# Kernel tuning notes

Hardware: AMD Instinct MI355X
Metric: run time of the kernel (lower is better)

## Reference

```python
import jax, jax.numpy as jnp
import numpy as np

B, C_IN, H, W = 2048, 192, 19, 19
G1, P1 = 32, 32

def setup_inputs() -> dict:
    key = jax.random.key(0)
    ks = jax.random.split(key, 10)
    inputs = jax.random.normal(ks[0], (B, C_IN, H, W), dtype=jnp.float32)
    # binary validity mask (most points valid), plus its per-sample sum
    mask = (jax.random.uniform(ks[1], (B, 1, H, W)) > 0.1).astype(jnp.float32)
    mask_sum_hw = jnp.sum(mask, axis=(2, 3), keepdims=True)  # [B,1,1,1]
    s = 0.05
    return {
        "inputs": inputs,
        "mask": mask,
        "mask_sum_hw": mask_sum_hw,
        "w1p": jax.random.normal(ks[2], (P1, C_IN), dtype=jnp.float32) * s,
        "b1p": jnp.zeros((P1,), jnp.float32),
        "w1g": jax.random.normal(ks[3], (G1, C_IN), dtype=jnp.float32) * s,
        "b1g": jnp.zeros((G1,), jnp.float32),
        "beta_g": jnp.zeros((1, G1, 1, 1), jnp.float32),
        "w_lin": jax.random.normal(ks[4], (P1, 3 * G1), dtype=jnp.float32) * s,
        "b_lin": jnp.zeros((P1,), jnp.float32),
        "beta2": jnp.zeros((1, P1, 1, 1), jnp.float32),
        "w2p": jax.random.normal(ks[5], (1, P1), dtype=jnp.float32) * s,
        "b2p": jnp.zeros((1,), jnp.float32),
    }

def _conv1x1(x, w, b):
    # x: [B,C,H,W], w: [O,C] -> [B,O,H,W]
    return jnp.einsum('bchw,oc->bohw', x, w) + b[None, :, None, None]

def _gpool(x, mask, mask_sum_hw):
    # x: [B,G,H,W]; returns [B,3G,1,1]
    off = (jnp.sqrt(mask_sum_hw) - 28.0) / 10.0
    mean = jnp.sum(x, axis=(2, 3), keepdims=True) / mask_sum_hw
    mx = jnp.max(x + (mask - 1.0), axis=(2, 3), keepdims=True)
    return jnp.concatenate([mean, mean * off, mx], axis=1)

def reference(inputs, mask, mask_sum_hw, w1p, b1p, w1g, b1g, beta_g,
              w_lin, b_lin, beta2, w2p, b2p):
    b, _, h, w = inputs.shape
    outp = _conv1x1(inputs, w1p, b1p)                      # [B,P1,H,W]
    outg = _conv1x1(inputs, w1g, b1g)                      # [B,G1,H,W]
    outg = (outg + beta_g) * mask                          # NormMask (no gamma)
    outg = jax.nn.gelu(outg, approximate=False)            # torch GELU = exact erf
    outg = _gpool(outg, mask, mask_sum_hw)                 # [B,3G1,1,1]
    outg = outg.reshape(b, -1) @ w_lin.T + b_lin           # [B,P1]
    outp = outp + outg[:, :, None, None]
    outp = (outp + beta2) * mask                           # NormMask
    outp = jax.nn.gelu(outp, approximate=False)
    outp = _conv1x1(outp, w2p, b2p)                        # [B,1,H,W]
    outp = outp - (1.0 - mask) * 5000.0
    outp = jax.nn.log_softmax(outp.reshape(b, -1), axis=1)
    return outp.reshape(b, h, w)
```

## Files before the change

kernel.cpp:

```cpp
#include <hip/hip_runtime.h>
#include <math.h>

#define NB   2048
#define CIN  192
#define HW   361
#define NTH  512
#define WPAD 200

typedef float f32x4 __attribute__((ext_vector_type(4)));
typedef short s16x8 __attribute__((ext_vector_type(8)));

__device__ __forceinline__ unsigned short f2bf(float f) {
    unsigned int u = __float_as_uint(f);
    u += 0x7FFFu + ((u >> 16) & 1u);
    return (unsigned short)(u >> 16);
}

__device__ __forceinline__ float gelu_exact(float x) {
    return 0.5f * x * (1.0f + erff(x * 0.70710678118654752f));
}

__global__ __launch_bounds__(NTH)
void policy_head_mfma(const float* __restrict__ inputs,
                      const float* __restrict__ mask,
                      const float* __restrict__ mask_sum,
                      const float* __restrict__ w1p, const float* __restrict__ b1p,
                      const float* __restrict__ w1g, const float* __restrict__ b1g,
                      const float* __restrict__ beta_g,
                      const float* __restrict__ w_lin, const float* __restrict__ b_lin,
                      const float* __restrict__ beta2,
                      const float* __restrict__ w2p, const float* __restrict__ b2p,
                      float* __restrict__ out) {
    __shared__ unsigned short wlds[64 * WPAD];
    __shared__ float small[160];
    __shared__ float redA[32 * 8];
    __shared__ float redB[32 * 8];
    __shared__ float pooled[96];
    __shared__ float linout[32];

    const int tid = threadIdx.x;
    const int b   = blockIdx.x;

    for (int i = tid; i < 64 * CIN; i += NTH) {
        int o = i / CIN, c = i - o * CIN;
        float wv = (o < 32) ? w1p[o * CIN + c] : w1g[(o - 32) * CIN + c];
        wlds[o * WPAD + c] = f2bf(wv);
    }
    if (tid < 32)       small[tid] = b1p[tid];
    else if (tid < 64)  small[tid] = b1g[tid - 32];
    else if (tid < 96)  small[tid] = beta_g[tid - 64];
    else if (tid < 128) small[tid] = beta2[tid - 96];
    else if (tid < 160) small[tid] = w2p[tid - 128];
    __syncthreads();

    const int w    = tid >> 6;
    const int lane = tid & 63;
    const int g4   = lane >> 4;
    const int c16  = lane & 15;

    int   px[3], pxc[3];
    float mv[3];
    bool  valid[3];
    #pragma unroll
    for (int nt = 0; nt < 3; ++nt) {
        px[nt]    = w * 48 + nt * 16 + c16;
        valid[nt] = (px[nt] < HW);
        pxc[nt]   = valid[nt] ? px[nt] : (HW - 1);
        mv[nt]    = valid[nt] ? mask[(size_t)b * HW + px[nt]] : 0.f;
    }

    const float* xb = inputs + (size_t)b * (CIN * HW);

    f32x4 acc[4][3];
    #pragma unroll
    for (int mt = 0; mt < 4; ++mt)
        #pragma unroll
        for (int nt = 0; nt < 3; ++nt)
            acc[mt][nt] = (f32x4){0.f, 0.f, 0.f, 0.f};

    for (int kk = 0; kk < 6; ++kk) {
        s16x8 a[4];
        #pragma unroll
        for (int mt = 0; mt < 4; ++mt)
            a[mt] = *(const s16x8*)&wlds[(mt * 16 + c16) * WPAD + kk * 32 + 8 * g4];

        #pragma unroll
        for (int nt = 0; nt < 3; ++nt) {
            const float* xp = xb + (size_t)(kk * 32 + 8 * g4) * HW + pxc[nt];
            float xv[8];
            #pragma unroll
            for (int i = 0; i < 8; ++i) xv[i] = xp[i * HW];
            s16x8 bf;
            #pragma unroll
            for (int i = 0; i < 8; ++i) bf[i] = (short)f2bf(xv[i]);
            #pragma unroll
            for (int mt = 0; mt < 4; ++mt)
                acc[mt][nt] = __builtin_amdgcn_mfma_f32_16x16x32_bf16(a[mt], bf, acc[mt][nt], 0, 0, 0);
        }
    }

    const float ms  = mask_sum[b];
    const float off = (sqrtf(ms) - 28.0f) * 0.1f;

    #pragma unroll
    for (int mt = 2; mt < 4; ++mt) {
        #pragma unroll
        for (int r = 0; r < 4; ++r) {
            int og = (mt - 2) * 16 + g4 * 4 + r;
            float bb = small[32 + og] + small[64 + og];
            float s = 0.f, mx = -1e30f;
            #pragma unroll
            for (int nt = 0; nt < 3; ++nt) {
                float v = gelu_exact((acc[mt][nt][r] + bb) * mv[nt]);
                if (!valid[nt]) v = 0.f;
                s += v;
                float cand = valid[nt] ? (v + mv[nt] - 1.f) : -1e30f;
                mx = fmaxf(mx, cand);
            }
            #pragma unroll
            for (int o = 1; o < 16; o <<= 1) {
                s += __shfl_xor(s, o, 64);
                mx = fmaxf(mx, __shfl_xor(mx, o, 64));
            }
            if (c16 == 0) { redA[og * 8 + w] = s; redB[og * 8 + w] = mx; }
        }
    }
    __syncthreads();

    if (tid < 32) {
        float s = 0.f, mx = -1e30f;
        #pragma unroll
        for (int j = 0; j < 8; ++j) {
            s += redA[tid * 8 + j];
            mx = fmaxf(mx, redB[tid * 8 + j]);
        }
        float mean = s / ms;
        pooled[tid]      = mean;
        pooled[32 + tid] = mean * off;
        pooled[64 + tid] = mx;
    }
    __syncthreads();

    if (tid < 32) {
        float a = b_lin[tid];
        #pragma unroll
        for (int j = 0; j < 96; ++j) a = fmaf(pooled[j], w_lin[tid * 96 + j], a);
        linout[tid] = a;
    }
    __syncthreads();

    float pv[3] = {0.f, 0.f, 0.f};
    #pragma unroll
    for (int mt = 0; mt < 2; ++mt) {
        #pragma unroll
        for (int r = 0; r < 4; ++r) {
            int op = mt * 16 + g4 * 4 + r;
            float bb = small[op] + linout[op] + small[96 + op];
            float wo = small[128 + op];
            #pragma unroll
            for (int nt = 0; nt < 3; ++nt)
                pv[nt] += gelu_exact((acc[mt][nt][r] + bb) * mv[nt]) * wo;
        }
    }
    const float b2 = b2p[0];
    float logit[3];
    #pragma unroll
    for (int nt = 0; nt < 3; ++nt) {
        float t = pv[nt];
        t += __shfl_xor(t, 16, 64);
        t += __shfl_xor(t, 32, 64);
        logit[nt] = t + b2 - (1.f - mv[nt]) * 5000.f;
    }

    float lmax = -1e30f;
    #pragma unroll
    for (int nt = 0; nt < 3; ++nt)
        if (valid[nt]) lmax = fmaxf(lmax, logit[nt]);
    #pragma unroll
    for (int o = 1; o < 64; o <<= 1) lmax = fmaxf(lmax, __shfl_xor(lmax, o, 64));
    if (lane == 0) redA[w] = lmax;
    __syncthreads();
    float gmax = -1e30f;
    #pragma unroll
    for (int j = 0; j < 8; ++j) gmax = fmaxf(gmax, redA[j]);

    float es = 0.f;
    #pragma unroll
    for (int nt = 0; nt < 3; ++nt)
        if (valid[nt] && g4 == 0) es += expf(logit[nt] - gmax);
    #pragma unroll
    for (int o = 1; o < 64; o <<= 1) es += __shfl_xor(es, o, 64);
    if (lane == 0) redB[w] = es;
    __syncthreads();
    float tot = 0.f;
    #pragma unroll
    for (int j = 0; j < 8; ++j) tot += redB[j];
    const float lt = logf(tot) + gmax;

    if (g4 == 0) {
        #pragma unroll
        for (int nt = 0; nt < 3; ++nt)
            if (valid[nt]) out[(size_t)b * HW + px[nt]] = logit[nt] - lt;
    }
}

extern "C" void kernel_launch(void* const* d_in, const int* in_sizes, int n_in,
                              void* d_out, int out_size, void* d_ws, size_t ws_size,
                              hipStream_t stream) {
    const float* inputs   = (const float*)d_in[0];
    const float* mask     = (const float*)d_in[1];
    const float* mask_sum = (const float*)d_in[2];
    const float* w1p      = (const float*)d_in[3];
    const float* b1p      = (const float*)d_in[4];
    const float* w1g      = (const float*)d_in[5];
    const float* b1g      = (const float*)d_in[6];
    const float* beta_g   = (const float*)d_in[7];
    const float* w_lin    = (const float*)d_in[8];
    const float* b_lin    = (const float*)d_in[9];
    const float* beta2    = (const float*)d_in[10];
    const float* w2p      = (const float*)d_in[11];
    const float* b2p      = (const float*)d_in[12];
    float* out = (float*)d_out;

    policy_head_mfma<<<dim3(NB), dim3(NTH), 0, stream>>>(
        inputs, mask, mask_sum, w1p, b1p, w1g, b1g, beta_g,
        w_lin, b_lin, beta2, w2p, b2p, out);
}
```

Measured before the change: 176.7 us.

## Prefetch next K-slice of inputs, use tanh GELU approximation and fast intrinsics

Software-pipelines the global loads of input activations: each iteration converts the previously loaded slice to bf16 and issues the loads for the next slice before the MFMAs, to hide memory latency. It also replaces the exact erf GELU with a tanh-style approximation via __expf, switches expf/logf to fast intrinsics, uses the library bf16 conversion, and sets launch bounds to 4 blocks per CU. The GELU approximation changes numerics relative to the exact erf reference, and the extra register buffer may raise register pressure. The last iteration issues a redundant reload of slice 0.

```diff
diff --git a/kernel.cpp b/kernel.cpp
--- a/kernel.cpp
+++ b/kernel.cpp
@@ -1,4 +1,5 @@
 #include <hip/hip_runtime.h>
+#include <hip/hip_bf16.h>
 #include <math.h>
 
 #define NB   2048
@@ -10,17 +11,22 @@
 typedef float f32x4 __attribute__((ext_vector_type(4)));
 typedef short s16x8 __attribute__((ext_vector_type(8)));
 
-__device__ __forceinline__ unsigned short f2bf(float f) {
-    unsigned int u = __float_as_uint(f);
-    u += 0x7FFFu + ((u >> 16) & 1u);
-    return (unsigned short)(u >> 16);
-}
-
-__device__ __forceinline__ float gelu_exact(float x) {
-    return 0.5f * x * (1.0f + erff(x * 0.70710678118654752f));
-}
-
-__global__ __launch_bounds__(NTH)
+__device__ __forceinline__ short f2bf_bits(float f) {
+    __hip_bfloat16 h = __float2bfloat16(f);
+    short s;
+    __builtin_memcpy(&s, &h, sizeof(s));
+    return s;
+}
+
+__device__ __forceinline__ float gelu_fast(float x) {
+    float inner = x * fmaf(0.044715f, x * x, 1.0f);
+    float t = 1.5957691216057308f * inner;
+    if (t > 40.f) return x;
+    float e = __expf(t);
+    return x * (e / (e + 1.0f));
+}
+
+__global__ __launch_bounds__(NTH, 4)
 void policy_head_mfma(const float* __restrict__ inputs,
                       const float* __restrict__ mask,
                       const float* __restrict__ mask_sum,
@@ -44,7 +50,7 @@
     for (int i = tid; i < 64 * CIN; i += NTH) {
         int o = i / CIN, c = i - o * CIN;
         float wv = (o < 32) ? w1p[o * CIN + c] : w1g[(o - 32) * CIN + c];
-        wlds[o * WPAD + c] = f2bf(wv);
+        wlds[o * WPAD + c] = (unsigned short)f2bf_bits(wv);
     }
     if (tid < 32)       small[tid] = b1p[tid];
     else if (tid < 64)  small[tid] = b1g[tid - 32];
@@ -57,6 +63,7 @@
     const int lane = tid & 63;
     const int g4   = lane >> 4;
     const int c16  = lane & 15;
+    const int krow = 8 * g4;
 
     int   px[3], pxc[3];
     float mv[3];
@@ -71,6 +78,16 @@
 
     const float* xb = inputs + (size_t)b * (CIN * HW);
 
+    auto loadx = [&](float (&xv)[3][8], int kk) {
+        const float* xk = xb + (size_t)(kk * 32 + krow) * HW;
+        #pragma unroll
+        for (int nt = 0; nt < 3; ++nt) {
+            const float* xp = xk + pxc[nt];
+            #pragma unroll
+            for (int i = 0; i < 8; ++i) xv[nt][i] = xp[i * HW];
+        }
+    };
+
     f32x4 acc[4][3];
     #pragma unroll
     for (int mt = 0; mt < 4; ++mt)
@@ -78,25 +95,30 @@
         for (int nt = 0; nt < 3; ++nt)
             acc[mt][nt] = (f32x4){0.f, 0.f, 0.f, 0.f};
 
+    float xv[3][8];
+    loadx(xv, 0);
+
     for (int kk = 0; kk < 6; ++kk) {
+        s16x8 bfr[3];
+        #pragma unroll
+        for (int nt = 0; nt < 3; ++nt)
+            #pragma unroll
+            for (int i = 0; i < 8; ++i)
+                bfr[nt][i] = f2bf_bits(xv[nt][i]);
+
+        int kkn = (kk < 5) ? kk + 1 : 0;
+        loadx(xv, kkn);
+
         s16x8 a[4];
         #pragma unroll
         for (int mt = 0; mt < 4; ++mt)
-            a[mt] = *(const s16x8*)&wlds[(mt * 16 + c16) * WPAD + kk * 32 + 8 * g4];
-
-        #pragma unroll
-        for (int nt = 0; nt < 3; ++nt) {
-            const float* xp = xb + (size_t)(kk * 32 + 8 * g4) * HW + pxc[nt];
-            float xv[8];
-            #pragma unroll
-            for (int i = 0; i < 8; ++i) xv[i] = xp[i * HW];
-            s16x8 bf;
-            #pragma unroll
-            for (int i = 0; i < 8; ++i) bf[i] = (short)f2bf(xv[i]);
+            a[mt] = *(const s16x8*)&wlds[(mt * 16 + c16) * WPAD + kk * 32 + krow];
+
+        #pragma unroll
+        for (int nt = 0; nt < 3; ++nt)
             #pragma unroll
             for (int mt = 0; mt < 4; ++mt)
-                acc[mt][nt] = __builtin_amdgcn_mfma_f32_16x16x32_bf16(a[mt], bf, acc[mt][nt], 0, 0, 0);
-        }
+                acc[mt][nt] = __builtin_amdgcn_mfma_f32_16x16x32_bf16(a[mt], bfr[nt], acc[mt][nt], 0, 0, 0);
     }
 
     const float ms  = mask_sum[b];
@@ -111,7 +133,7 @@
             float s = 0.f, mx = -1e30f;
             #pragma unroll
             for (int nt = 0; nt < 3; ++nt) {
-                float v = gelu_exact((acc[mt][nt][r] + bb) * mv[nt]);
+                float v = gelu_fast((acc[mt][nt][r] + bb) * mv[nt]);
                 if (!valid[nt]) v = 0.f;
                 s += v;
                 float cand = valid[nt] ? (v + mv[nt] - 1.f) : -1e30f;
@@ -159,7 +181,7 @@
             float wo = small[128 + op];
             #pragma unroll
             for (int nt = 0; nt < 3; ++nt)
-                pv[nt] += gelu_exact((acc[mt][nt][r] + bb) * mv[nt]) * wo;
+                pv[nt] += gelu_fast((acc[mt][nt][r] + bb) * mv[nt]) * wo;
         }
     }
     const float b2 = b2p[0];
@@ -187,7 +209,7 @@
     float es = 0.f;
     #pragma unroll
     for (int nt = 0; nt < 3; ++nt)
-        if (valid[nt] && g4 == 0) es += expf(logit[nt] - gmax);
+        if (valid[nt] && g4 == 0) es += __expf(logit[nt] - gmax);
     #pragma unroll
     for (int o = 1; o < 64; o <<= 1) es += __shfl_xor(es, o, 64);
     if (lane == 0) redB[w] = es;
@@ -195,7 +217,7 @@
     float tot = 0.f;
     #pragma unroll
     for (int j = 0; j < 8; ++j) tot += redB[j];
-    const float lt = logf(tot) + gmax;
+    const float lt = __logf(tot) + gmax;
 
     if (g4 == 0) {
         #pragma unroll
```

Result: faster. 156.7 us (-11.4%).
